# Performance work log

Hardware: AMD Instinct MI355X
Metric: run time of the kernel (lower is better)

## Reference

```python
import jax, jax.numpy as jnp
import numpy as np

EPS = 1e-6
NUM_HEADS = 16

def _rmsnorm(h, w):
    hf = h.astype(jnp.float32)
    var = jnp.mean(hf * hf, axis=-1, keepdims=True)
    return (w * (hf * jax.lax.rsqrt(var + EPS))).astype(h.dtype)

def _rotary(t, cos, sin):
    # t: [B,N,H,hd]; cos/sin: [N, hd//2]
    tf = t.astype(jnp.float32)
    tr = tf[..., 0::2]
    ti = tf[..., 1::2]
    c = cos[None, :, None, :]
    s = sin[None, :, None, :]
    out_r = tr * c - ti * s
    out_i = tr * s + ti * c
    out = jnp.stack([out_r, out_i], axis=-1).reshape(t.shape)
    return out.astype(t.dtype)

def setup_inputs() -> dict:
    key = jax.random.key(0)
    ks = jax.random.split(key, 8)
    B, N, C = 2, 2048, 1024
    hd = C // NUM_HEADS
    x = jax.random.normal(ks[0], (B, N, C), jnp.float32)
    qkv_w = jax.random.normal(ks[1], (3 * C, C), jnp.float32) * (C ** -0.5)
    q_norm_w = jnp.ones((hd,), jnp.float32)
    k_norm_w = jnp.ones((hd,), jnp.float32)
    proj_w = jax.random.normal(ks[2], (C, C), jnp.float32) * (C ** -0.5)
    proj_b = jnp.zeros((C,), jnp.float32)
    # rotary freqs_cis = exp(i * theta): unit-magnitude cos/sin
    inv_freq = 1.0 / (10000.0 ** (jnp.arange(0, hd, 2, dtype=jnp.float32) / hd))
    ang = jnp.arange(N, dtype=jnp.float32)[:, None] * inv_freq[None, :]
    pos_cos = jnp.cos(ang)
    pos_sin = jnp.sin(ang)
    mask = jnp.tril(jnp.ones((N, N), dtype=bool))
    return {"x": x, "qkv_w": qkv_w, "q_norm_w": q_norm_w, "k_norm_w": k_norm_w,
            "proj_w": proj_w, "proj_b": proj_b, "pos_cos": pos_cos,
            "pos_sin": pos_sin, "mask": mask}

def reference(x, qkv_w, q_norm_w, k_norm_w, proj_w, proj_b, pos_cos, pos_sin, mask):
    B, N, C = x.shape
    H = NUM_HEADS
    hd = C // H
    qkv = (x @ qkv_w.T).reshape(B, N, 3, H, hd)
    q, k, v = qkv[:, :, 0], qkv[:, :, 1], qkv[:, :, 2]  # [B,N,H,hd]
    q = _rmsnorm(q, q_norm_w)
    k = _rmsnorm(k, k_norm_w)
    q = _rotary(q, pos_cos, pos_sin)
    k = _rotary(k, pos_cos, pos_sin)
    q = q.transpose(0, 2, 1, 3)  # [B,H,N,hd]
    k = k.transpose(0, 2, 1, 3)
    v = v.transpose(0, 2, 1, 3)
    scale = hd ** -0.5
    scores = jnp.einsum('bhqd,bhkd->bhqk', q, k) * scale
    scores = jnp.where(mask[None, None, :, :], scores, jnp.float32(-1e30))
    attn = jax.nn.softmax(scores, axis=-1)
    out = jnp.einsum('bhqk,bhkd->bhqd', attn, v)
    out = out.transpose(0, 2, 1, 3).reshape(B, N, C)
    return out @ proj_w.T + proj_b
```

## Files before the change

kernel.cpp:

```cpp
#include <hip/hip_runtime.h>

using u16 = unsigned short;
using short4v = __attribute__((ext_vector_type(4))) short;
using short8 = __attribute__((ext_vector_type(8))) short;
using floatx4 = __attribute__((ext_vector_type(4))) float;

__device__ __forceinline__ float bf2f(u16 h) {
  union { unsigned int u; float f; } v;
  v.u = ((unsigned int)h) << 16;
  return v.f;
}
__device__ __forceinline__ u16 f2bf(float f) {
  union { float f; unsigned int u; } v;
  v.f = f;
  unsigned int u = v.u;
  return (u16)((u + 0x7FFFu + ((u >> 16) & 1u)) >> 16);
}
__device__ __forceinline__ u16 f2bf_rtz(float f) {
  union { float f; unsigned int u; } v;
  v.f = f;
  return (u16)(v.u >> 16);
}

typedef const __attribute__((address_space(1))) unsigned int* gas_t;
typedef __attribute__((address_space(3))) unsigned int* las_t;
__device__ __forceinline__ void gl_lds16(const u16* g, u16* l) {
  __builtin_amdgcn_global_load_lds((gas_t)(const void*)g, (las_t)(void*)l, 16,
                                   0, 0);
}

#define QSCALE 0.180336880111f
#define EXPBIAS 23.0831206542f

__global__ __launch_bounds__(256) void cvt_all(
    const float* __restrict__ x, const float* __restrict__ wq,
    const float* __restrict__ wp, u16* __restrict__ xb, u16* __restrict__ wqb,
    u16* __restrict__ wpb) {
  int i = blockIdx.x * 256 + threadIdx.x;
  const float* src;
  u16* dst;
  int off;
  if (i < 1048576) {
    src = x; dst = xb; off = i;
  } else if (i < 1048576 + 786432) {
    src = wq; dst = wqb; off = i - 1048576;
  } else {
    src = wp; dst = wpb; off = i - 1835008;
  }
  float4 v = ((const float4*)src)[off];
  ushort4 o;
  o.x = f2bf(v.x);
  o.y = f2bf(v.y);
  o.z = f2bf(v.z);
  o.w = f2bf(v.w);
  ((ushort4*)dst)[off] = o;
}

template <int BIAS, int OUTBF16>
__global__ __launch_bounds__(256) void gemm_nt(
    const u16* __restrict__ A, const u16* __restrict__ B,
    const float* __restrict__ bias, void* __restrict__ Cout,
    int M, int N, int K) {
  __shared__ u16 As[128 * 32];
  __shared__ u16 Bs[128 * 32];
  const int tid = threadIdx.x;
  const int lane = tid & 63;
  const int wave = tid >> 6;
  const int col = lane & 15;
  const int quad = lane >> 4;
  const int bm = blockIdx.y * 128;
  const int bn = blockIdx.x * 128;
  const int wm = (wave >> 1) * 64;
  const int wn = (wave & 1) * 64;

  floatx4 acc[4][4] = {};

  for (int kb = 0; kb < K; kb += 32) {
    __syncthreads();
#pragma unroll
    for (int i = 0; i < 2; i++) {
      const int c = i * 256 + tid;
      const int row = c >> 2;
      const int kc = (c & 3) * 8;
      gl_lds16(A + (size_t)(bm + row) * K + kb + kc, (u16*)As + c * 8);
      gl_lds16(B + (size_t)(bn + row) * K + kb + kc, (u16*)Bs + c * 8);
    }
    __syncthreads();

    short8 af[4], bfr[4];
#pragma unroll
    for (int i = 0; i < 4; i++)
      af[i] = *(const short8*)(As + (wm + i * 16 + col) * 32 + quad * 8);
#pragma unroll
    for (int i = 0; i < 4; i++)
      bfr[i] = *(const short8*)(Bs + (wn + i * 16 + col) * 32 + quad * 8);
#pragma unroll
    for (int mi = 0; mi < 4; mi++)
#pragma unroll
      for (int ni = 0; ni < 4; ni++)
        acc[mi][ni] = __builtin_amdgcn_mfma_f32_16x16x32_bf16(
            af[mi], bfr[ni], acc[mi][ni], 0, 0, 0);
  }

#pragma unroll
  for (int mi = 0; mi < 4; mi++) {
#pragma unroll
    for (int ni = 0; ni < 4; ni++) {
#pragma unroll
      for (int r = 0; r < 4; r++) {
        int row = bm + wm + mi * 16 + quad * 4 + r;
        int c = bn + wn + ni * 16 + col;
        float v = acc[mi][ni][r];
        if (BIAS) v += bias[c];
        if (OUTBF16)
          ((u16*)Cout)[(size_t)row * N + c] = f2bf(v);
        else
          ((float*)Cout)[(size_t)row * N + c] = v;
      }
    }
  }
}

__global__ __launch_bounds__(256) void rope_v(
    const u16* __restrict__ qkv, const float* __restrict__ qw,
    const float* __restrict__ kw, const float* __restrict__ pcos,
    const float* __restrict__ psin, u16* __restrict__ Qb,
    u16* __restrict__ Kb, u16* __restrict__ Vt) {
  __shared__ u16 T[64 * 68];
  const int bh = blockIdx.x;
  const int n0 = blockIdx.y * 64;
  const int b = bh >> 4, h = bh & 15;
  const int tid = threadIdx.x;
  const int lane = tid & 63;
  const int wave = tid >> 6;

  const float qwl = qw[lane];
  const float kwl = kw[lane];
  for (int tt = 0; tt < 16; tt++) {
    const int n = n0 + wave * 16 + tt;
    const int t = b * 2048 + n;
    const u16* base = qkv + (size_t)t * 3072 + h * 64 + lane;
    float qv = bf2f(base[0]);
    float kv = bf2f(base[1024]);

    float sq = qv * qv, sk = kv * kv;
#pragma unroll
    for (int off = 32; off; off >>= 1) {
      sq += __shfl_xor(sq, off);
      sk += __shfl_xor(sk, off);
    }
    float qn = qv * rsqrtf(sq * (1.0f / 64.0f) + 1e-6f) * qwl;
    float kn = kv * rsqrtf(sk * (1.0f / 64.0f) + 1e-6f) * kwl;

    const int i = lane >> 1;
    const float c = pcos[n * 32 + i];
    const float s = psin[n * 32 + i];
    float qp = __shfl_xor(qn, 1);
    float kp = __shfl_xor(kn, 1);
    float qr, kr;
    if (lane & 1) {
      qr = qp * s + qn * c;
      kr = kp * s + kn * c;
    } else {
      qr = qn * c - qp * s;
      kr = kn * c - kp * s;
    }
    qr *= QSCALE;

    const size_t o = ((size_t)bh * 2048 + n) * 64 + lane;
    Qb[o] = f2bf(qr);
    Kb[o] = f2bf(kr);
  }

  const int q = tid & 7;
  const int r = tid >> 3;
#pragma unroll
  for (int rr = r; rr < 64; rr += 32) {
    short8 v = *(const short8*)(qkv + (size_t)(b * 2048 + n0 + rr) * 3072 +
                                2048 + h * 64 + q * 8);
    *(short8*)&T[rr * 68 + q * 8] = v;
  }
  __syncthreads();
#pragma unroll
  for (int dd = r; dd < 64; dd += 32) {
    short8 o;
#pragma unroll
    for (int j = 0; j < 8; j++) o[j] = T[(q * 8 + j) * 68 + dd];
    *(short8*)(Vt + (size_t)(bh * 64 + dd) * 2048 + n0 + q * 8) = o;
  }
}

#define PSTR 72
__global__ __launch_bounds__(256) void attn_flash(
    const u16* __restrict__ Q, const u16* __restrict__ Kk,
    const u16* __restrict__ Vt, u16* __restrict__ O) {
  __shared__ u16 Ks[2][64 * 32];
  __shared__ u16 Vs[2][64 * 32];
  __shared__ u16 Pb[4][16 * PSTR];
  const int id = blockIdx.x;
  const int bh = id & 31;
  const int tile = 31 - (id >> 5);
  const int tid = threadIdx.x;
  const int lane = tid & 63;
  const int wave = tid >> 6;
  const int col = lane & 15;
  const int quad = lane >> 4;
  const int srow = tid >> 2;
  const int spc = (tid & 3) * 8;

  const u16* Qh = Q + (size_t)bh * 2048 * 64;
  const u16* Kh = Kk + (size_t)bh * 2048 * 64;
  const u16* Vh = Vt + (size_t)bh * 64 * 2048;
  const int b = bh >> 4, h = bh & 15;

  const int q0 = tile * 64 + wave * 16;

  short8 aq[2];
#pragma unroll
  for (int ks = 0; ks < 2; ks++)
    aq[ks] = *(const short8*)(Qh + (size_t)(q0 + col) * 64 + ks * 32 + quad * 8);

  floatx4 accO[4] = {};
  float ll = 0.0f;
  const int nsteps = tile + 1;

  for (int kt = 0; kt < nsteps; kt++) {
    const int j0 = kt * 64;
    __syncthreads();
#pragma unroll
    for (int half = 0; half < 2; half++) {
      gl_lds16(Kh + (size_t)(j0 + srow) * 64 + half * 32 + spc,
               &Ks[half][0] + tid * 8);
      gl_lds16(Vh + (size_t)srow * 2048 + j0 + half * 32 + spc,
               &Vs[half][0] + tid * 8);
    }
    __syncthreads();

    floatx4 s[4] = {};
#pragma unroll
    for (int nt = 0; nt < 4; nt++) {
#pragma unroll
      for (int ks = 0; ks < 2; ks++) {
        short8 bk = *(const short8*)&Ks[ks][(nt * 16 + col) * 32 + quad * 8];
        s[nt] =
            __builtin_amdgcn_mfma_f32_16x16x32_bf16(bk, aq[ks], s[nt], 0, 0, 0);
      }
    }

    if (j0 + 63 <= q0) {
#pragma unroll
      for (int nt = 0; nt < 4; nt++) {
        short4v pk;
#pragma unroll
        for (int r = 0; r < 4; r++) {
          float pv = exp2f(s[nt][r] - EXPBIAS);
          ll += pv;
          pk[r] = (short)f2bf_rtz(pv);
        }
        *(short4v*)&Pb[wave][col * PSTR + nt * 16 + quad * 4] = pk;
      }
    } else {
      const int qg = q0 + col;
#pragma unroll
      for (int nt = 0; nt < 4; nt++) {
        const int jgb = j0 + nt * 16 + quad * 4;
        short4v pk;
#pragma unroll
        for (int r = 0; r < 4; r++) {
          float pv = (jgb + r <= qg) ? exp2f(s[nt][r] - EXPBIAS) : 0.0f;
          ll += pv;
          pk[r] = (short)f2bf_rtz(pv);
        }
        *(short4v*)&Pb[wave][col * PSTR + nt * 16 + quad * 4] = pk;
      }
    }

    short8 ap[2];
#pragma unroll
    for (int kf = 0; kf < 2; kf++)
      ap[kf] = *(const short8*)&Pb[wave][col * PSTR + kf * 32 + quad * 8];
#pragma unroll
    for (int nt = 0; nt < 4; nt++) {
#pragma unroll
      for (int kf = 0; kf < 2; kf++) {
        short8 bv = *(const short8*)&Vs[kf][(nt * 16 + col) * 32 + quad * 8];
        accO[nt] =
            __builtin_amdgcn_mfma_f32_16x16x32_bf16(ap[kf], bv, accO[nt], 0, 0, 0);
      }
    }
  }

  ll += __shfl_xor(ll, 16);
  ll += __shfl_xor(ll, 32);
  float lrec[4];
#pragma unroll
  for (int r = 0; r < 4; r++) lrec[r] = 1.0f / __shfl(ll, quad * 4 + r);

#pragma unroll
  for (int nt = 0; nt < 4; nt++) {
#pragma unroll
    for (int r = 0; r < 4; r++) {
      int qg = q0 + quad * 4 + r;
      int d = nt * 16 + col;
      O[((size_t)(b * 2048 + qg) * 16 + h) * 64 + d] =
          f2bf(accO[nt][r] * lrec[r]);
    }
  }
}

extern "C" void kernel_launch(void* const* d_in, const int* in_sizes, int n_in,
                              void* d_out, int out_size, void* d_ws,
                              size_t ws_size, hipStream_t stream) {
  const float* x = (const float*)d_in[0];
  const float* qkv_w = (const float*)d_in[1];
  const float* q_norm_w = (const float*)d_in[2];
  const float* k_norm_w = (const float*)d_in[3];
  const float* proj_w = (const float*)d_in[4];
  const float* proj_b = (const float*)d_in[5];
  const float* pos_cos = (const float*)d_in[6];
  const float* pos_sin = (const float*)d_in[7];

  char* ws = (char*)d_ws;
  u16* xb = (u16*)ws;
  u16* wqkvb = (u16*)(ws + 8388608);
  u16* wprojb = (u16*)(ws + 14680064);
  u16* qkv = (u16*)(ws + 16777216);
  u16* Qb = (u16*)(ws + 41943040);
  u16* Kb = (u16*)(ws + 50331648);
  u16* Vt = (u16*)(ws + 58720256);
  u16* AO = (u16*)(ws + 67108864);

  cvt_all<<<8192, 256, 0, stream>>>(x, qkv_w, proj_w, xb, wqkvb, wprojb);

  gemm_nt<0, 1><<<dim3(3072 / 128, 4096 / 128), 256, 0, stream>>>(
      xb, wqkvb, nullptr, qkv, 4096, 3072, 1024);

  rope_v<<<dim3(32, 32), 256, 0, stream>>>(qkv, q_norm_w, k_norm_w, pos_cos,
                                           pos_sin, Qb, Kb, Vt);

  attn_flash<<<dim3(1024), 256, 0, stream>>>(Qb, Kb, Vt, AO);

  gemm_nt<1, 0><<<dim3(1024 / 128, 4096 / 128), 256, 0, stream>>>(
      AO, wprojb, proj_b, (float*)d_out, 4096, 1024, 1024);
}
```

Baseline: 225.2 us.

## Process 128 query rows per attention block to reuse K/V tiles

Each wave of the flash attention kernel now handles two 16-row query subtiles, so a block covers 128 queries and the grid halves to 512 blocks. Every K/V tile loaded into shared memory feeds twice as many MFMAs, cutting global-to-LDS traffic and barrier overhead per unit of work. Subtiles that lie fully past the causal diagonal skip their softmax and PV work, but the QK MFMAs still run for both. The costs are higher register use (launch bounds now request 4 blocks per CU), fewer blocks to spread over the CUs, and coarser causal load imbalance.

```diff
diff --git a/kernel.cpp b/kernel.cpp
--- a/kernel.cpp
+++ b/kernel.cpp
@@ -190,16 +190,16 @@
   }
 }
 
-#define PSTR 72
-__global__ __launch_bounds__(256) void attn_flash(
+#define PSTR 68
+__global__ __launch_bounds__(256, 4) void attn_flash(
     const u16* __restrict__ Q, const u16* __restrict__ Kk,
     const u16* __restrict__ Vt, u16* __restrict__ O) {
   __shared__ u16 Ks[2][64 * 32];
   __shared__ u16 Vs[2][64 * 32];
-  __shared__ u16 Pb[4][16 * PSTR];
+  __shared__ u16 Pb[4][32 * PSTR];
   const int id = blockIdx.x;
   const int bh = id & 31;
-  const int tile = 31 - (id >> 5);
+  const int tile = 15 - (id >> 5);
   const int tid = threadIdx.x;
   const int lane = tid & 63;
   const int wave = tid >> 6;
@@ -213,16 +213,19 @@
   const u16* Vh = Vt + (size_t)bh * 64 * 2048;
   const int b = bh >> 4, h = bh & 15;
 
-  const int q0 = tile * 64 + wave * 16;
-
-  short8 aq[2];
-#pragma unroll
-  for (int ks = 0; ks < 2; ks++)
-    aq[ks] = *(const short8*)(Qh + (size_t)(q0 + col) * 64 + ks * 32 + quad * 8);
-
-  floatx4 accO[4] = {};
-  float ll = 0.0f;
-  const int nsteps = tile + 1;
+  const int qw = tile * 128 + wave * 32;
+
+  short8 aq[2][2];
+#pragma unroll
+  for (int mt = 0; mt < 2; mt++)
+#pragma unroll
+    for (int ks = 0; ks < 2; ks++)
+      aq[mt][ks] = *(const short8*)(Qh + (size_t)(qw + mt * 16 + col) * 64 +
+                                    ks * 32 + quad * 8);
+
+  floatx4 accO[2][4] = {};
+  float ll[2] = {0.f, 0.f};
+  const int nsteps = 2 * tile + 2;
 
   for (int kt = 0; kt < nsteps; kt++) {
     const int j0 = kt * 64;
@@ -236,74 +239,96 @@
     }
     __syncthreads();
 
-    floatx4 s[4] = {};
+    const bool act0 = j0 <= qw + 15;
+    const bool act1 = j0 <= qw + 31;
+
+    floatx4 s[2][4] = {};
 #pragma unroll
     for (int nt = 0; nt < 4; nt++) {
 #pragma unroll
       for (int ks = 0; ks < 2; ks++) {
         short8 bk = *(const short8*)&Ks[ks][(nt * 16 + col) * 32 + quad * 8];
-        s[nt] =
-            __builtin_amdgcn_mfma_f32_16x16x32_bf16(bk, aq[ks], s[nt], 0, 0, 0);
-      }
-    }
-
-    if (j0 + 63 <= q0) {
-#pragma unroll
-      for (int nt = 0; nt < 4; nt++) {
-        short4v pk;
-#pragma unroll
-        for (int r = 0; r < 4; r++) {
-          float pv = exp2f(s[nt][r] - EXPBIAS);
-          ll += pv;
-          pk[r] = (short)f2bf_rtz(pv);
+        s[0][nt] = __builtin_amdgcn_mfma_f32_16x16x32_bf16(bk, aq[0][ks],
+                                                           s[0][nt], 0, 0, 0);
+        s[1][nt] = __builtin_amdgcn_mfma_f32_16x16x32_bf16(bk, aq[1][ks],
+                                                           s[1][nt], 0, 0, 0);
+      }
+    }
+
+#pragma unroll
+    for (int mt = 0; mt < 2; mt++) {
+      if (!(mt ? act1 : act0)) continue;
+      const int q0m = qw + mt * 16;
+      if (j0 + 63 <= q0m) {
+#pragma unroll
+        for (int nt = 0; nt < 4; nt++) {
+          short4v pk;
+#pragma unroll
+          for (int r = 0; r < 4; r++) {
+            float pv = exp2f(s[mt][nt][r] - EXPBIAS);
+            ll[mt] += pv;
+            pk[r] = (short)f2bf_rtz(pv);
+          }
+          *(short4v*)&Pb[wave][(mt * 16 + col) * PSTR + nt * 16 + quad * 4] = pk;
         }
-        *(short4v*)&Pb[wave][col * PSTR + nt * 16 + quad * 4] = pk;
-      }
-    } else {
-      const int qg = q0 + col;
-#pragma unroll
-      for (int nt = 0; nt < 4; nt++) {
-        const int jgb = j0 + nt * 16 + quad * 4;
-        short4v pk;
-#pragma unroll
-        for (int r = 0; r < 4; r++) {
-          float pv = (jgb + r <= qg) ? exp2f(s[nt][r] - EXPBIAS) : 0.0f;
-          ll += pv;
-          pk[r] = (short)f2bf_rtz(pv);
+      } else {
+        const int qg = q0m + col;
+#pragma unroll
+        for (int nt = 0; nt < 4; nt++) {
+          const int jgb = j0 + nt * 16 + quad * 4;
+          short4v pk;
+#pragma unroll
+          for (int r = 0; r < 4; r++) {
+            float pv = (jgb + r <= qg) ? exp2f(s[mt][nt][r] - EXPBIAS) : 0.0f;
+            ll[mt] += pv;
+            pk[r] = (short)f2bf_rtz(pv);
+          }
+          *(short4v*)&Pb[wave][(mt * 16 + col) * PSTR + nt * 16 + quad * 4] = pk;
         }
-        *(short4v*)&Pb[wave][col * PSTR + nt * 16 + quad * 4] = pk;
-      }
-    }
-
-    short8 ap[2];
-#pragma unroll
-    for (int kf = 0; kf < 2; kf++)
-      ap[kf] = *(const short8*)&Pb[wave][col * PSTR + kf * 32 + quad * 8];
+      }
+    }
+
+    short8 ap[2][2];
+#pragma unroll
+    for (int mt = 0; mt < 2; mt++)
+      if (mt ? act1 : act0) {
+#pragma unroll
+        for (int kf = 0; kf < 2; kf++)
+          ap[mt][kf] = *(const short8*)&Pb[wave][(mt * 16 + col) * PSTR +
+                                                 kf * 32 + quad * 8];
+      }
 #pragma unroll
     for (int nt = 0; nt < 4; nt++) {
 #pragma unroll
       for (int kf = 0; kf < 2; kf++) {
         short8 bv = *(const short8*)&Vs[kf][(nt * 16 + col) * 32 + quad * 8];
-        accO[nt] =
-            __builtin_amdgcn_mfma_f32_16x16x32_bf16(ap[kf], bv, accO[nt], 0, 0, 0);
-      }
-    }
-  }
-
-  ll += __shfl_xor(ll, 16);
-  ll += __shfl_xor(ll, 32);
-  float lrec[4];
-#pragma unroll
-  for (int r = 0; r < 4; r++) lrec[r] = 1.0f / __shfl(ll, quad * 4 + r);
-
-#pragma unroll
-  for (int nt = 0; nt < 4; nt++) {
-#pragma unroll
-    for (int r = 0; r < 4; r++) {
-      int qg = q0 + quad * 4 + r;
-      int d = nt * 16 + col;
-      O[((size_t)(b * 2048 + qg) * 16 + h) * 64 + d] =
-          f2bf(accO[nt][r] * lrec[r]);
+        if (act0)
+          accO[0][nt] = __builtin_amdgcn_mfma_f32_16x16x32_bf16(
+              ap[0][kf], bv, accO[0][nt], 0, 0, 0);
+        if (act1)
+          accO[1][nt] = __builtin_amdgcn_mfma_f32_16x16x32_bf16(
+              ap[1][kf], bv, accO[1][nt], 0, 0, 0);
+      }
+    }
+  }
+
+#pragma unroll
+  for (int mt = 0; mt < 2; mt++) {
+    float l = ll[mt];
+    l += __shfl_xor(l, 16);
+    l += __shfl_xor(l, 32);
+    float lrec[4];
+#pragma unroll
+    for (int r = 0; r < 4; r++) lrec[r] = 1.0f / __shfl(l, quad * 4 + r);
+#pragma unroll
+    for (int nt = 0; nt < 4; nt++) {
+#pragma unroll
+      for (int r = 0; r < 4; r++) {
+        int qg = qw + mt * 16 + quad * 4 + r;
+        int d = nt * 16 + col;
+        O[((size_t)(b * 2048 + qg) * 16 + h) * 64 + d] =
+            f2bf(accO[mt][nt][r] * lrec[r]);
+      }
     }
   }
 }
@@ -338,7 +363,7 @@
   rope_v<<<dim3(32, 32), 256, 0, stream>>>(qkv, q_norm_w, k_norm_w, pos_cos,
                                            pos_sin, Qb, Kb, Vt);
 
-  attn_flash<<<dim3(1024), 256, 0, stream>>>(Qb, Kb, Vt, AO);
+  attn_flash<<<dim3(512), 256, 0, stream>>>(Qb, Kb, Vt, AO);
 
   gemm_nt<1, 0><<<dim3(1024 / 128, 4096 / 128), 256, 0, stream>>>(
       AO, wprojb, proj_b, (float*)d_out, 4096, 1024, 1024);
```

Result: slower. 239.5 us (+6.4%).
